# Kernel tuning notes

Measured on AMD Instinct MI355X. Metric: run time of the kernel, lower is better.

The kernel has to match this reference:

```python
import jax, jax.numpy as jnp
import numpy as np

IN_FEATURES = 1024
OUT_FEATURES = 1024
NUM_GRIDS = 8
GRID_MIN, GRID_MAX = -2.0, 2.0
DENOM = (GRID_MAX - GRID_MIN) / (NUM_GRIDS - 1)
LN_EPS = 1e-5
GRID = jnp.linspace(GRID_MIN, GRID_MAX, NUM_GRIDS)


def setup_inputs() -> dict:
    key = jax.random.key(0)
    k_x, k_sw, k_bw = jax.random.split(key, 3)
    N = 8192
    x = jax.random.normal(k_x, (N, IN_FEATURES), dtype=jnp.float32)
    ln_gamma = jnp.ones((IN_FEATURES,), dtype=jnp.float32)
    ln_beta = jnp.zeros((IN_FEATURES,), dtype=jnp.float32)
    # trunc_normal(std=0.1) approximated by scaled normal
    spline_w = 0.1 * jax.random.normal(k_sw, (OUT_FEATURES, IN_FEATURES * NUM_GRIDS), dtype=jnp.float32)
    base_w = jax.random.normal(k_bw, (OUT_FEATURES, IN_FEATURES), dtype=jnp.float32) * (1.0 / np.sqrt(IN_FEATURES))
    base_b = jnp.zeros((OUT_FEATURES,), dtype=jnp.float32)
    return {"x": x, "ln_gamma": ln_gamma, "ln_beta": ln_beta,
            "spline_w": spline_w, "base_w": base_w, "base_b": base_b}


def reference(x, ln_gamma, ln_beta, spline_w, base_w, base_b):
    # LayerNorm over last dim
    mu = jnp.mean(x, axis=-1, keepdims=True)
    var = jnp.var(x, axis=-1, keepdims=True)
    xn = (x - mu) * jax.lax.rsqrt(var + LN_EPS) * ln_gamma + ln_beta
    # RBF basis: [N, in, G]
    basis = jnp.exp(-jnp.square((xn[..., None] - GRID) / DENOM))
    basis = basis.reshape(x.shape[0], IN_FEATURES * NUM_GRIDS)
    y = jnp.einsum('nk,ok->no', basis, spline_w)
    y = y + jnp.einsum('nd,od->no', jax.nn.silu(x), base_w) + base_b
    return y
```

## Files before the change

### kernel.cpp

```cpp
#include <hip/hip_runtime.h>
#include <hip/hip_bf16.h>
#include <stdint.h>

#define IN_F 1024
#define OUT_F 1024
#define NG 8
#define KSPLINE 8192
#define KDIM 9216
#define M_ROWS 8192
#define LOG2E 1.4426950408889634f
#define KC 2.1019642153762872f

#define A_BLOCKS (M_ROWS / 4)
#define W_BLOCKS ((OUT_F * 2304) / 256)

using half4v = __attribute__((ext_vector_type(4))) _Float16;
using half8  = __attribute__((ext_vector_type(8))) _Float16;
using f32x4  = __attribute__((ext_vector_type(4))) float;

#define AS1 __attribute__((address_space(1)))
#define AS3 __attribute__((address_space(3)))

__global__ __launch_bounds__(256) void prep_kernel(
        const float* __restrict__ x, const float* __restrict__ gamma,
        const float* __restrict__ beta, const float* __restrict__ sw,
        const float* __restrict__ bw, _Float16* __restrict__ A,
        _Float16* __restrict__ W) {
    if (blockIdx.x >= A_BLOCKS) {
        int idx = (blockIdx.x - A_BLOCKS) * 256 + threadIdx.x;
        int o   = idx / 2304;
        int k4  = idx - o * 2304;
        float4 v;
        if (k4 < 2048) v = ((const float4*)sw)[(size_t)o * 2048 + k4];
        else           v = ((const float4*)bw)[(size_t)o * 256 + (k4 - 2048)];
        half4v h = { (_Float16)v.x, (_Float16)v.y, (_Float16)v.z, (_Float16)v.w };
        *(half4v*)(W + (size_t)idx * 4) = h;
        return;
    }
    const int wave = threadIdx.x >> 6, lane = threadIdx.x & 63;
    const int row = blockIdx.x * 4 + wave;
    const float* xr = x + (size_t)row * IN_F;

    float xv[16];
    float s = 0.0f, s2 = 0.0f;
#pragma unroll
    for (int j = 0; j < 16; ++j) {
        float v = xr[j * 64 + lane];
        xv[j] = v;
        s += v;
        s2 += v * v;
    }
#pragma unroll
    for (int off = 32; off > 0; off >>= 1) {
        s  += __shfl_xor(s, off);
        s2 += __shfl_xor(s2, off);
    }
    float mu   = s * (1.0f / IN_F);
    float var  = s2 * (1.0f / IN_F) - mu * mu;
    float rstd = rsqrtf(var + 1e-5f);

    const float cq[8] = {
        -2.0000000f * KC, -1.4285715f * KC, -0.8571429f * KC, -0.2857143f * KC,
         0.2857143f * KC,  0.8571429f * KC,  1.4285715f * KC,  2.0000000f * KC };

    _Float16* Arow = A + (size_t)row * KDIM;
    half8* basis_out = (half8*)Arow;
    _Float16* silu_out = Arow + KSPLINE;
#pragma unroll
    for (int j = 0; j < 16; ++j) {
        int f = j * 64 + lane;
        float xs = xv[j];
        float xq = ((xs - mu) * rstd * gamma[f] + beta[f]) * KC;
        half8 h;
#pragma unroll
        for (int g = 0; g < 8; ++g) {
            float v = xq - cq[g];
            h[g] = (_Float16)exp2f(-(v * v));
        }
        basis_out[f] = h;
        silu_out[f] = (_Float16)(xs / (1.0f + exp2f(-xs * LOG2E)));
    }
}

__global__ __launch_bounds__(256, 2) void gemm_kernel(
        const _Float16* __restrict__ A, const _Float16* __restrict__ W,
        const float* __restrict__ bias, float* __restrict__ C) {
    __shared__ alignas(16) _Float16 As[4][128 * 32];
    __shared__ alignas(16) _Float16 Bs[4][128 * 32];
    const int bm = blockIdx.x, bn = blockIdx.y;
    const int tid = threadIdx.x;
    const int wave = tid >> 6, lane = tid & 63;
    const int wm = wave >> 1, wn = wave & 1;

    f32x4 acc[4][4] = {};

    const _Float16* gAj[2];
    const _Float16* gBj[2];
    int ldsOff[2];
#pragma unroll
    for (int j = 0; j < 2; ++j) {
        int chunk = wave * 128 + j * 64 + lane;
        int r  = chunk >> 2;
        int c8 = (chunk & 3) * 8;
        gAj[j] = A + (size_t)(bm * 128 + r) * KDIM + c8;
        gBj[j] = W + (size_t)(bn * 128 + r) * KDIM + c8;
        ldsOff[j] = chunk * 8;
    }

    const int lm = lane & 15;
    const int lk = (lane >> 4) * 8;

    for (int kt = 0; kt < KDIM / 128; ++kt) {
        __syncthreads();
#pragma unroll
        for (int h = 0; h < 4; ++h)
#pragma unroll
            for (int j = 0; j < 2; ++j) {
                __builtin_amdgcn_global_load_lds(
                    (const AS1 void*)(gAj[j] + kt * 128 + h * 32),
                    (AS3 void*)(&As[h][0] + ldsOff[j]), 16, 0, 0);
                __builtin_amdgcn_global_load_lds(
                    (const AS1 void*)(gBj[j] + kt * 128 + h * 32),
                    (AS3 void*)(&Bs[h][0] + ldsOff[j]), 16, 0, 0);
            }
        __syncthreads();

#pragma unroll
        for (int h = 0; h < 4; ++h) {
            half8 a[4], b[4];
#pragma unroll
            for (int i = 0; i < 4; ++i) {
                a[i] = *(const half8*)(&As[h][0] + (wm * 64 + i * 16 + lm) * 32 + lk);
                b[i] = *(const half8*)(&Bs[h][0] + (wn * 64 + i * 16 + lm) * 32 + lk);
            }
#pragma unroll
            for (int mi = 0; mi < 4; ++mi)
#pragma unroll
                for (int ni = 0; ni < 4; ++ni)
                    acc[mi][ni] = __builtin_amdgcn_mfma_f32_16x16x32_f16(
                        a[mi], b[ni], acc[mi][ni], 0, 0, 0);
        }
    }

    const int cn = lane & 15;
    const int rm = (lane >> 4) * 4;
#pragma unroll
    for (int ni = 0; ni < 4; ++ni) {
        int col = bn * 128 + wn * 64 + ni * 16 + cn;
        float bv = bias[col];
#pragma unroll
        for (int mi = 0; mi < 4; ++mi) {
            int row = bm * 128 + wm * 64 + mi * 16 + rm;
            float* Cp = C + (size_t)row * OUT_F + col;
#pragma unroll
            for (int r = 0; r < 4; ++r)
                Cp[(size_t)r * OUT_F] = acc[mi][ni][r] + bv;
        }
    }
}

extern "C" void kernel_launch(void* const* d_in, const int* in_sizes, int n_in,
                              void* d_out, int out_size, void* d_ws, size_t ws_size,
                              hipStream_t stream) {
    const float* x     = (const float*)d_in[0];
    const float* gamma = (const float*)d_in[1];
    const float* beta  = (const float*)d_in[2];
    const float* sw    = (const float*)d_in[3];
    const float* bw    = (const float*)d_in[4];
    const float* bb    = (const float*)d_in[5];
    float* out = (float*)d_out;

    char* ws = (char*)d_ws;
    _Float16* Wb = (_Float16*)ws;
    _Float16* Ab = (_Float16*)(ws + (size_t)OUT_F * KDIM * 2);

    prep_kernel<<<A_BLOCKS + W_BLOCKS, 256, 0, stream>>>(
        x, gamma, beta, sw, bw, Ab, Wb);
    gemm_kernel<<<dim3(M_ROWS / 128, OUT_F / 128), 256, 0, stream>>>(
        Ab, Wb, bb, out);
}
```

Before: 296.2 us.

## Rewrite GEMM with 256x128 tiles, double-buffered swizzled LDS and 8 waves

The GEMM moves to 512-thread blocks computing 256x128 output tiles with a K step of 64. Global-to-LDS loads are double-buffered, using XOR-swizzled LDS layouts to avoid bank conflicts and explicit waitcnt, barrier and setprio scheduling so MFMA work overlaps the next tile's loads. The prep kernel also switches to float4 loads and stores. Costs are 96 KB of dynamic LDS, heavier register pressure and more barriers per iteration.

```diff
diff --git a/kernel.cpp b/kernel.cpp
--- a/kernel.cpp
+++ b/kernel.cpp
@@ -13,6 +13,8 @@
 
 #define A_BLOCKS (M_ROWS / 4)
 #define W_BLOCKS ((OUT_F * 2304) / 256)
+
+#define RB (KDIM * 2)
 
 using half4v = __attribute__((ext_vector_type(4))) _Float16;
 using half8  = __attribute__((ext_vector_type(8))) _Float16;
@@ -39,16 +41,16 @@
     }
     const int wave = threadIdx.x >> 6, lane = threadIdx.x & 63;
     const int row = blockIdx.x * 4 + wave;
-    const float* xr = x + (size_t)row * IN_F;
-
-    float xv[16];
+    const float4* xr = (const float4*)(x + (size_t)row * IN_F);
+
+    float4 xv[4];
     float s = 0.0f, s2 = 0.0f;
 #pragma unroll
-    for (int j = 0; j < 16; ++j) {
-        float v = xr[j * 64 + lane];
+    for (int j = 0; j < 4; ++j) {
+        float4 v = xr[j * 64 + lane];
         xv[j] = v;
-        s += v;
-        s2 += v * v;
+        s  += v.x + v.y + v.z + v.w;
+        s2 += v.x * v.x + v.y * v.y + v.z * v.z + v.w * v.w;
     }
 #pragma unroll
     for (int off = 32; off > 0; off >>= 1) {
@@ -66,91 +68,147 @@
     _Float16* Arow = A + (size_t)row * KDIM;
     half8* basis_out = (half8*)Arow;
     _Float16* silu_out = Arow + KSPLINE;
-#pragma unroll
-    for (int j = 0; j < 16; ++j) {
-        int f = j * 64 + lane;
-        float xs = xv[j];
-        float xq = ((xs - mu) * rstd * gamma[f] + beta[f]) * KC;
-        half8 h;
-#pragma unroll
-        for (int g = 0; g < 8; ++g) {
-            float v = xq - cq[g];
-            h[g] = (_Float16)exp2f(-(v * v));
-        }
-        basis_out[f] = h;
-        silu_out[f] = (_Float16)(xs / (1.0f + exp2f(-xs * LOG2E)));
+    const float4* g4 = (const float4*)gamma;
+    const float4* b4 = (const float4*)beta;
+#pragma unroll
+    for (int j = 0; j < 4; ++j) {
+        int idx = j * 64 + lane;
+        float4 g = g4[idx], bt = b4[idx];
+        float xs4[4] = { xv[j].x, xv[j].y, xv[j].z, xv[j].w };
+        float gg4[4] = { g.x, g.y, g.z, g.w };
+        float bb4[4] = { bt.x, bt.y, bt.z, bt.w };
+        half4v sil;
+#pragma unroll
+        for (int c = 0; c < 4; ++c) {
+            float xs = xs4[c];
+            float xq = ((xs - mu) * rstd * gg4[c] + bb4[c]) * KC;
+            half8 h;
+#pragma unroll
+            for (int gi = 0; gi < 8; ++gi) {
+                float v = xq - cq[gi];
+                h[gi] = (_Float16)exp2f(-(v * v));
+            }
+            basis_out[idx * 4 + c] = h;
+            sil[c] = (_Float16)(xs / (1.0f + exp2f(-xs * LOG2E)));
+        }
+        *(half4v*)(silu_out + idx * 4) = sil;
     }
 }
 
-__global__ __launch_bounds__(256, 2) void gemm_kernel(
+__global__ __launch_bounds__(512, 2) void gemm_kernel(
         const _Float16* __restrict__ A, const _Float16* __restrict__ W,
         const float* __restrict__ bias, float* __restrict__ C) {
-    __shared__ alignas(16) _Float16 As[4][128 * 32];
-    __shared__ alignas(16) _Float16 Bs[4][128 * 32];
-    const int bm = blockIdx.x, bn = blockIdx.y;
-    const int tid = threadIdx.x;
+    extern __shared__ __align__(16) char smem[];
+    const int tid  = threadIdx.x;
     const int wave = tid >> 6, lane = tid & 63;
     const int wm = wave >> 1, wn = wave & 1;
+    const int bm = blockIdx.x, bn = blockIdx.y;
+
+    const int l8 = lane >> 3;
+    const int srcswz = ((lane & 7) ^ l8) << 4;
+    const char* pA = (const char*)A + (size_t)(bm * 256 + wave * 32 + l8) * RB + srcswz;
+    const char* pB = (const char*)W + (size_t)(bn * 128 + wave * 16 + l8) * RB + srcswz;
+    const int dstA = wave * 4096;
+    const int dstB = wave * 2048;
+
+    const int lm   = lane & 15;
+    const int hi16 = (lane >> 4) << 4;
+    const int rowA = wm * 64 + lm;
+    const int swzA = (rowA & 7) << 4;
+    const int aoff0 = rowA * 128 + (hi16 ^ swzA);
+    const int aoff1 = rowA * 128 + ((64 | hi16) ^ swzA);
+    const int rowB = wn * 64 + lm;
+    const int swzB = (rowB & 7) << 4;
+    const int boff0 = rowB * 128 + (hi16 ^ swzB);
+    const int boff1 = rowB * 128 + ((64 | hi16) ^ swzB);
 
     f32x4 acc[4][4] = {};
 
-    const _Float16* gAj[2];
-    const _Float16* gBj[2];
-    int ldsOff[2];
-#pragma unroll
-    for (int j = 0; j < 2; ++j) {
-        int chunk = wave * 128 + j * 64 + lane;
-        int r  = chunk >> 2;
-        int c8 = (chunk & 3) * 8;
-        gAj[j] = A + (size_t)(bm * 128 + r) * KDIM + c8;
-        gBj[j] = W + (size_t)(bn * 128 + r) * KDIM + c8;
-        ldsOff[j] = chunk * 8;
-    }
-
-    const int lm = lane & 15;
-    const int lk = (lane >> 4) * 8;
-
-    for (int kt = 0; kt < KDIM / 128; ++kt) {
-        __syncthreads();
-#pragma unroll
-        for (int h = 0; h < 4; ++h)
-#pragma unroll
-            for (int j = 0; j < 2; ++j) {
-                __builtin_amdgcn_global_load_lds(
-                    (const AS1 void*)(gAj[j] + kt * 128 + h * 32),
-                    (AS3 void*)(&As[h][0] + ldsOff[j]), 16, 0, 0);
-                __builtin_amdgcn_global_load_lds(
-                    (const AS1 void*)(gBj[j] + kt * 128 + h * 32),
-                    (AS3 void*)(&Bs[h][0] + ldsOff[j]), 16, 0, 0);
-            }
-        __syncthreads();
-
-#pragma unroll
-        for (int h = 0; h < 4; ++h) {
-            half8 a[4], b[4];
-#pragma unroll
-            for (int i = 0; i < 4; ++i) {
-                a[i] = *(const half8*)(&As[h][0] + (wm * 64 + i * 16 + lm) * 32 + lk);
-                b[i] = *(const half8*)(&Bs[h][0] + (wn * 64 + i * 16 + lm) * 32 + lk);
-            }
-#pragma unroll
-            for (int mi = 0; mi < 4; ++mi)
-#pragma unroll
-                for (int ni = 0; ni < 4; ++ni)
-                    acc[mi][ni] = __builtin_amdgcn_mfma_f32_16x16x32_f16(
-                        a[mi], b[ni], acc[mi][ni], 0, 0, 0);
-        }
-    }
-
-    const int cn = lane & 15;
-    const int rm = (lane >> 4) * 4;
+#pragma unroll
+    for (int j = 0; j < 4; ++j)
+        __builtin_amdgcn_global_load_lds((const AS1 void*)(pA + (size_t)j * 8 * RB),
+            (AS3 void*)(smem + dstA + j * 1024), 16, 0, 0);
+#pragma unroll
+    for (int j = 0; j < 2; ++j)
+        __builtin_amdgcn_global_load_lds((const AS1 void*)(pB + (size_t)j * 8 * RB),
+            (AS3 void*)(smem + 65536 + dstB + j * 1024), 16, 0, 0);
+
+    const int NT = KDIM / 64;
+    for (int kt = 0; kt < NT; ++kt) {
+        const int cur = kt & 1;
+        char* sA  = smem + cur * 32768;
+        char* sAn = smem + (cur ^ 1) * 32768;
+        char* sB  = smem + 65536 + cur * 16384;
+        char* sBn = smem + 65536 + (cur ^ 1) * 16384;
+
+        if (kt + 1 < NT) {
+            const char* pAn = pA + (size_t)(kt + 1) * 128;
+#pragma unroll
+            for (int j = 0; j < 4; ++j)
+                __builtin_amdgcn_global_load_lds((const AS1 void*)(pAn + (size_t)j * 8 * RB),
+                    (AS3 void*)(sAn + dstA + j * 1024), 16, 0, 0);
+            asm volatile("s_waitcnt vmcnt(4)" ::: "memory");
+        } else {
+            asm volatile("s_waitcnt vmcnt(0)" ::: "memory");
+        }
+        __builtin_amdgcn_s_barrier();
+
+        half8 b[4][2];
+#pragma unroll
+        for (int ni = 0; ni < 4; ++ni) {
+            b[ni][0] = *(const half8*)(sB + (boff0 + ni * 2048));
+            b[ni][1] = *(const half8*)(sB + (boff1 + ni * 2048));
+        }
+        half8 a0 = *(const half8*)(sA + aoff0);
+        half8 a1 = *(const half8*)(sA + aoff1);
+        if (kt + 1 < NT) {
+            const char* pBn = pB + (size_t)(kt + 1) * 128;
+#pragma unroll
+            for (int j = 0; j < 2; ++j)
+                __builtin_amdgcn_global_load_lds((const AS1 void*)(pBn + (size_t)j * 8 * RB),
+                    (AS3 void*)(sBn + dstB + j * 1024), 16, 0, 0);
+        }
+        __builtin_amdgcn_s_barrier();
+        asm volatile("s_waitcnt lgkmcnt(0)" ::: "memory");
+        __builtin_amdgcn_sched_barrier(0);
+        __builtin_amdgcn_s_setprio(1);
+#pragma unroll
+        for (int ni = 0; ni < 4; ++ni)
+            acc[0][ni] = __builtin_amdgcn_mfma_f32_16x16x32_f16(a0, b[ni][0], acc[0][ni], 0, 0, 0);
+#pragma unroll
+        for (int ni = 0; ni < 4; ++ni)
+            acc[0][ni] = __builtin_amdgcn_mfma_f32_16x16x32_f16(a1, b[ni][1], acc[0][ni], 0, 0, 0);
+        __builtin_amdgcn_s_setprio(0);
+        __builtin_amdgcn_s_barrier();
+
+#pragma unroll
+        for (int p = 1; p < 4; ++p) {
+            half8 c0 = *(const half8*)(sA + (aoff0 + p * 2048));
+            half8 c1 = *(const half8*)(sA + (aoff1 + p * 2048));
+            __builtin_amdgcn_s_barrier();
+            asm volatile("s_waitcnt lgkmcnt(0)" ::: "memory");
+            __builtin_amdgcn_sched_barrier(0);
+            __builtin_amdgcn_s_setprio(1);
+#pragma unroll
+            for (int ni = 0; ni < 4; ++ni)
+                acc[p][ni] = __builtin_amdgcn_mfma_f32_16x16x32_f16(c0, b[ni][0], acc[p][ni], 0, 0, 0);
+#pragma unroll
+            for (int ni = 0; ni < 4; ++ni)
+                acc[p][ni] = __builtin_amdgcn_mfma_f32_16x16x32_f16(c1, b[ni][1], acc[p][ni], 0, 0, 0);
+            __builtin_amdgcn_s_setprio(0);
+            __builtin_amdgcn_s_barrier();
+        }
+    }
+
+    const int cn  = lane & 15;
+    const int rm4 = (lane >> 4) * 4;
 #pragma unroll
     for (int ni = 0; ni < 4; ++ni) {
         int col = bn * 128 + wn * 64 + ni * 16 + cn;
         float bv = bias[col];
 #pragma unroll
         for (int mi = 0; mi < 4; ++mi) {
-            int row = bm * 128 + wm * 64 + mi * 16 + rm;
+            int row = bm * 256 + wm * 64 + mi * 16 + rm4;
             float* Cp = C + (size_t)row * OUT_F + col;
 #pragma unroll
             for (int r = 0; r < 4; ++r)
@@ -174,8 +232,15 @@
     _Float16* Wb = (_Float16*)ws;
     _Float16* Ab = (_Float16*)(ws + (size_t)OUT_F * KDIM * 2);
 
+    static int s_attr = 0;
+    if (!s_attr) {
+        hipFuncSetAttribute(reinterpret_cast<const void*>(gemm_kernel),
+                            hipFuncAttributeMaxDynamicSharedMemorySize, 98304);
+        s_attr = 1;
+    }
+
     prep_kernel<<<A_BLOCKS + W_BLOCKS, 256, 0, stream>>>(
         x, gamma, beta, sw, bw, Ab, Wb);
-    gemm_kernel<<<dim3(M_ROWS / 128, OUT_F / 128), 256, 0, stream>>>(
+    gemm_kernel<<<dim3(M_ROWS / 256, OUT_F / 128), 512, 98304, stream>>>(
         Ab, Wb, bb, out);
 }
```

New measurement: 311.5 us. 5.2% more time.

## Rewrite GEMM with 256x256 tiles, double-buffered swizzled LDS, split-K and XCD-aware mapping

Applied to the files above, without the earlier changes.

The GEMM moves to 512-thread blocks computing 256x256 output tiles. Loads go through global_load_lds into two 64 KB LDS buffers with an XOR swizzle, so the next K tile streams in while MFMAs run on the current one, with explicit waitcnt, barriers and setprio. Blocks are remapped across the 8 XCDs. When the workspace is large enough, K is split in two, and a separate reduce kernel adds the fp32 partial sums into the output. This is meant to raise data reuse and keep the CUs busy given the small number of large tiles, at the cost of an extra fp32 partial buffer and a reduction pass.

```diff
diff --git a/kernel.cpp b/kernel.cpp
--- a/kernel.cpp
+++ b/kernel.cpp
@@ -7,12 +7,14 @@
 #define NG 8
 #define KSPLINE 8192
 #define KDIM 9216
+#define KHALF 4608
 #define M_ROWS 8192
 #define LOG2E 1.4426950408889634f
 #define KC 2.1019642153762872f
 
 #define A_BLOCKS (M_ROWS / 4)
 #define W_BLOCKS ((OUT_F * 2304) / 256)
+#define RB (KDIM * 2)
 
 using half4v = __attribute__((ext_vector_type(4))) _Float16;
 using half8  = __attribute__((ext_vector_type(8))) _Float16;
@@ -82,80 +84,149 @@
     }
 }
 
-__global__ __launch_bounds__(256, 2) void gemm_kernel(
+__global__ __launch_bounds__(512, 2) void gemm_kernel(
         const _Float16* __restrict__ A, const _Float16* __restrict__ W,
-        const float* __restrict__ bias, float* __restrict__ C) {
-    __shared__ alignas(16) _Float16 As[4][128 * 32];
-    __shared__ alignas(16) _Float16 Bs[4][128 * 32];
-    const int bm = blockIdx.x, bn = blockIdx.y;
-    const int tid = threadIdx.x;
+        const float* __restrict__ bias, float* __restrict__ C,
+        float* __restrict__ P, int ntiles, int gpz) {
+    extern __shared__ __align__(16) char smem[];
+    const int tid  = threadIdx.x;
     const int wave = tid >> 6, lane = tid & 63;
-    const int wm = wave >> 1, wn = wave & 1;
-
-    f32x4 acc[4][4] = {};
-
-    const _Float16* gAj[2];
-    const _Float16* gBj[2];
-    int ldsOff[2];
-#pragma unroll
-    for (int j = 0; j < 2; ++j) {
-        int chunk = wave * 128 + j * 64 + lane;
-        int r  = chunk >> 2;
-        int c8 = (chunk & 3) * 8;
-        gAj[j] = A + (size_t)(bm * 128 + r) * KDIM + c8;
-        gBj[j] = W + (size_t)(bn * 128 + r) * KDIM + c8;
-        ldsOff[j] = chunk * 8;
-    }
-
-    const int lm = lane & 15;
-    const int lk = (lane >> 4) * 8;
-
-    for (int kt = 0; kt < KDIM / 128; ++kt) {
-        __syncthreads();
-#pragma unroll
-        for (int h = 0; h < 4; ++h)
-#pragma unroll
-            for (int j = 0; j < 2; ++j) {
-                __builtin_amdgcn_global_load_lds(
-                    (const AS1 void*)(gAj[j] + kt * 128 + h * 32),
-                    (AS3 void*)(&As[h][0] + ldsOff[j]), 16, 0, 0);
-                __builtin_amdgcn_global_load_lds(
-                    (const AS1 void*)(gBj[j] + kt * 128 + h * 32),
-                    (AS3 void*)(&Bs[h][0] + ldsOff[j]), 16, 0, 0);
-            }
-        __syncthreads();
-
-#pragma unroll
-        for (int h = 0; h < 4; ++h) {
-            half8 a[4], b[4];
-#pragma unroll
-            for (int i = 0; i < 4; ++i) {
-                a[i] = *(const half8*)(&As[h][0] + (wm * 64 + i * 16 + lm) * 32 + lk);
-                b[i] = *(const half8*)(&Bs[h][0] + (wn * 64 + i * 16 + lm) * 32 + lk);
-            }
-#pragma unroll
-            for (int mi = 0; mi < 4; ++mi)
-#pragma unroll
-                for (int ni = 0; ni < 4; ++ni)
-                    acc[mi][ni] = __builtin_amdgcn_mfma_f32_16x16x32_f16(
-                        a[mi], b[ni], acc[mi][ni], 0, 0, 0);
-        }
-    }
-
-    const int cn = lane & 15;
-    const int rm = (lane >> 4) * 4;
-#pragma unroll
-    for (int ni = 0; ni < 4; ++ni) {
-        int col = bn * 128 + wn * 64 + ni * 16 + cn;
-        float bv = bias[col];
-#pragma unroll
-        for (int mi = 0; mi < 4; ++mi) {
-            int row = bm * 128 + wm * 64 + mi * 16 + rm;
-            float* Cp = C + (size_t)row * OUT_F + col;
+    const int wm = wave >> 2, wn = wave & 3;
+
+    const int lb = blockIdx.x;
+    const int per_xcd = gridDim.x >> 5;
+    const int xcd = lb & 7, sl = lb >> 3;
+    const int g  = xcd * per_xcd + (sl >> 2);
+    const int bn = sl & 3;
+    const int bm = g / gpz;
+    const int z  = g - bm * gpz;
+
+    const int l8 = lane >> 3;
+    const int srcswz = ((lane & 7) ^ l8) << 4;
+    const char* pA = (const char*)A + (size_t)(bm * 256 + wave * 8 + l8) * RB
+                     + (size_t)z * (KHALF * 2) + srcswz;
+    const char* pB = (const char*)W + (size_t)(bn * 256 + wave * 8 + l8) * RB
+                     + (size_t)z * (KHALF * 2) + srcswz;
+    const int dstOff = wave * 1024;
+
+    const int lm  = lane & 15;
+    const int hi  = (lane >> 4) << 4;
+    const int swz = (lm & 7) << 4;
+    const int aoff0 = (wm * 128 + lm) * 128 + ((0  + hi) ^ swz);
+    const int aoff1 = (wm * 128 + lm) * 128 + ((64 + hi) ^ swz);
+    const int boff0 = 32768 + (wn * 64 + lm) * 128 + ((0  + hi) ^ swz);
+    const int boff1 = 32768 + (wn * 64 + lm) * 128 + ((64 + hi) ^ swz);
+
+    f32x4 acc[8][4] = {};
+
+#pragma unroll
+    for (int j = 0; j < 4; ++j) {
+        __builtin_amdgcn_global_load_lds((const AS1 void*)(pA + (size_t)j * 64 * RB),
+            (AS3 void*)(smem + j * 8192 + dstOff), 16, 0, 0);
+        __builtin_amdgcn_global_load_lds((const AS1 void*)(pB + (size_t)j * 64 * RB),
+            (AS3 void*)(smem + 32768 + j * 8192 + dstOff), 16, 0, 0);
+    }
+
+    for (int kt = 0; kt < ntiles; ++kt) {
+        char* sbuf = smem + (kt & 1) * 65536;
+        char* nbuf = smem + ((kt & 1) ^ 1) * 65536;
+
+        if (kt + 1 < ntiles) {
+            const size_t kb = (size_t)(kt + 1) * 128;
+#pragma unroll
+            for (int j = 0; j < 4; ++j) {
+                __builtin_amdgcn_global_load_lds((const AS1 void*)(pA + (size_t)j * 64 * RB + kb),
+                    (AS3 void*)(nbuf + j * 8192 + dstOff), 16, 0, 0);
+                __builtin_amdgcn_global_load_lds((const AS1 void*)(pB + (size_t)j * 64 * RB + kb),
+                    (AS3 void*)(nbuf + 32768 + j * 8192 + dstOff), 16, 0, 0);
+            }
+            asm volatile("s_waitcnt vmcnt(8)" ::: "memory");
+        } else {
+            asm volatile("s_waitcnt vmcnt(0)" ::: "memory");
+        }
+        __builtin_amdgcn_s_barrier();
+
+        half8 b[4][2];
+#pragma unroll
+        for (int nf = 0; nf < 4; ++nf) {
+            b[nf][0] = *(const half8*)(sbuf + boff0 + nf * 2048);
+            b[nf][1] = *(const half8*)(sbuf + boff1 + nf * 2048);
+        }
+        {
+            half8 a00 = *(const half8*)(sbuf + aoff0);
+            half8 a01 = *(const half8*)(sbuf + aoff1);
+            half8 a10 = *(const half8*)(sbuf + aoff0 + 2048);
+            half8 a11 = *(const half8*)(sbuf + aoff1 + 2048);
+            __builtin_amdgcn_s_barrier();
+            asm volatile("s_waitcnt lgkmcnt(0)" ::: "memory");
+            __builtin_amdgcn_sched_barrier(0);
+            __builtin_amdgcn_s_setprio(1);
+#pragma unroll
+            for (int nf = 0; nf < 4; ++nf) {
+                acc[0][nf] = __builtin_amdgcn_mfma_f32_16x16x32_f16(a00, b[nf][0], acc[0][nf], 0, 0, 0);
+                acc[1][nf] = __builtin_amdgcn_mfma_f32_16x16x32_f16(a10, b[nf][0], acc[1][nf], 0, 0, 0);
+            }
+#pragma unroll
+            for (int nf = 0; nf < 4; ++nf) {
+                acc[0][nf] = __builtin_amdgcn_mfma_f32_16x16x32_f16(a01, b[nf][1], acc[0][nf], 0, 0, 0);
+                acc[1][nf] = __builtin_amdgcn_mfma_f32_16x16x32_f16(a11, b[nf][1], acc[1][nf], 0, 0, 0);
+            }
+            __builtin_amdgcn_s_setprio(0);
+            __builtin_amdgcn_s_barrier();
+        }
+#pragma unroll
+        for (int p = 1; p < 4; ++p) {
+            half8 a00 = *(const half8*)(sbuf + aoff0 + (2 * p) * 2048);
+            half8 a01 = *(const half8*)(sbuf + aoff1 + (2 * p) * 2048);
+            half8 a10 = *(const half8*)(sbuf + aoff0 + (2 * p + 1) * 2048);
+            half8 a11 = *(const half8*)(sbuf + aoff1 + (2 * p + 1) * 2048);
+            __builtin_amdgcn_s_barrier();
+            asm volatile("s_waitcnt lgkmcnt(0)" ::: "memory");
+            __builtin_amdgcn_sched_barrier(0);
+            __builtin_amdgcn_s_setprio(1);
+#pragma unroll
+            for (int nf = 0; nf < 4; ++nf) {
+                acc[2*p][nf]   = __builtin_amdgcn_mfma_f32_16x16x32_f16(a00, b[nf][0], acc[2*p][nf], 0, 0, 0);
+                acc[2*p+1][nf] = __builtin_amdgcn_mfma_f32_16x16x32_f16(a10, b[nf][0], acc[2*p+1][nf], 0, 0, 0);
+            }
+#pragma unroll
+            for (int nf = 0; nf < 4; ++nf) {
+                acc[2*p][nf]   = __builtin_amdgcn_mfma_f32_16x16x32_f16(a01, b[nf][1], acc[2*p][nf], 0, 0, 0);
+                acc[2*p+1][nf] = __builtin_amdgcn_mfma_f32_16x16x32_f16(a11, b[nf][1], acc[2*p+1][nf], 0, 0, 0);
+            }
+            __builtin_amdgcn_s_setprio(0);
+            __builtin_amdgcn_s_barrier();
+        }
+    }
+
+    const int cn  = lane & 15;
+    const int rm4 = (lane >> 4) * 4;
+    float* dst = z ? P : C;
+#pragma unroll
+    for (int nf = 0; nf < 4; ++nf) {
+        int col = bn * 256 + wn * 64 + nf * 16 + cn;
+        float bv = z ? 0.0f : bias[col];
+#pragma unroll
+        for (int mf = 0; mf < 8; ++mf) {
+            int row = bm * 256 + wm * 128 + mf * 16 + rm4;
+            float* cp = dst + (size_t)row * OUT_F + col;
 #pragma unroll
             for (int r = 0; r < 4; ++r)
-                Cp[(size_t)r * OUT_F] = acc[mi][ni][r] + bv;
-        }
+                cp[(size_t)r * OUT_F] = acc[mf][nf][r] + bv;
+        }
+    }
+}
+
+__global__ __launch_bounds__(256) void reduce_kernel(float* __restrict__ C,
+        const float* __restrict__ P) {
+    const int n4 = M_ROWS * OUT_F / 4;
+    float4* c4 = (float4*)C;
+    const float4* p4 = (const float4*)P;
+    for (int i = blockIdx.x * 256 + threadIdx.x; i < n4; i += 2048 * 256) {
+        float4 a = c4[i];
+        float4 b = p4[i];
+        a.x += b.x; a.y += b.y; a.z += b.z; a.w += b.w;
+        c4[i] = a;
     }
 }
 
@@ -171,11 +242,28 @@
     float* out = (float*)d_out;
 
     char* ws = (char*)d_ws;
-    _Float16* Wb = (_Float16*)ws;
-    _Float16* Ab = (_Float16*)(ws + (size_t)OUT_F * KDIM * 2);
+    size_t offW = 0;
+    size_t offA = (size_t)OUT_F * KDIM * 2;
+    size_t offP = offA + (size_t)M_ROWS * KDIM * 2;
+    size_t need = offP + (size_t)M_ROWS * OUT_F * 4;
+    _Float16* Wb = (_Float16*)(ws + offW);
+    _Float16* Ab = (_Float16*)(ws + offA);
+    float*    Pb = (float*)(ws + offP);
+    const int split = (ws_size >= need);
+
+    static int s_attr = 0;
+    if (!s_attr) {
+        hipFuncSetAttribute(reinterpret_cast<const void*>(gemm_kernel),
+                            hipFuncAttributeMaxDynamicSharedMemorySize, 131072);
+        s_attr = 1;
+    }
 
     prep_kernel<<<A_BLOCKS + W_BLOCKS, 256, 0, stream>>>(
         x, gamma, beta, sw, bw, Ab, Wb);
-    gemm_kernel<<<dim3(M_ROWS / 128, OUT_F / 128), 256, 0, stream>>>(
-        Ab, Wb, bb, out);
-}
+    if (split) {
+        gemm_kernel<<<256, 512, 131072, stream>>>(Ab, Wb, bb, out, Pb, KHALF / 64, 2);
+        reduce_kernel<<<2048, 256, 0, stream>>>(out, Pb);
+    } else {
+        gemm_kernel<<<128, 512, 131072, stream>>>(Ab, Wb, bb, out, Pb, KDIM / 64, 1);
+    }
+}
```

Result: no change. 297.1 us (+0.3%).
